# Performance work log

Hardware: AMD Instinct MI355X
Metric: run time of the kernel (lower is better)

## Reference

```python
import jax, jax.numpy as jnp
import numpy as np

B, L, D, H, NL, V, W = 4, 2048, 512, 8, 4, 258, 8
HD = D // H


def setup_inputs() -> dict:
    key = jax.random.key(0)
    ks = jax.random.split(key, 12)
    s = 0.02
    x = jax.random.randint(ks[0], (B, L), 0, V, dtype=jnp.int32)
    patch_lengths = jnp.full((B, 256), W, dtype=jnp.int32)  # sum over patches == L
    emb = jax.random.normal(ks[1], (V, D), jnp.float32) * s
    ent_w = jax.random.normal(ks[2], (D, 1), jnp.float32) * s
    ent_b = jnp.zeros((D,), jnp.float32)
    qkv_w = jax.random.normal(ks[3], (NL, 3 * D, D), jnp.float32) * s
    qkv_b = jnp.zeros((NL, 3 * D), jnp.float32)
    ao_w = jax.random.normal(ks[4], (NL, D, D), jnp.float32) * s
    ao_b = jnp.zeros((NL, D), jnp.float32)
    ln1_s = jnp.ones((NL, D), jnp.float32)
    ln1_b = jnp.zeros((NL, D), jnp.float32)
    ln2_s = jnp.ones((NL, D), jnp.float32)
    ln2_b = jnp.zeros((NL, D), jnp.float32)
    ff1_w = jax.random.normal(ks[5], (NL, 4 * D, D), jnp.float32) * s
    ff1_b = jnp.zeros((NL, 4 * D), jnp.float32)
    ff2_w = jax.random.normal(ks[6], (NL, D, 4 * D), jnp.float32) * s
    ff2_b = jnp.zeros((NL, D), jnp.float32)
    out_w = jax.random.normal(ks[7], (V, D), jnp.float32) * s
    return {"emb": emb, "ent_w": ent_w, "ent_b": ent_b, "qkv_w": qkv_w,
            "qkv_b": qkv_b, "ao_w": ao_w, "ao_b": ao_b, "ln1_s": ln1_s,
            "ln1_b": ln1_b, "ln2_s": ln2_s, "ln2_b": ln2_b, "ff1_w": ff1_w,
            "ff1_b": ff1_b, "ff2_w": ff2_w, "ff2_b": ff2_b, "out_w": out_w,
            "x": x, "patch_lengths": patch_lengths}


def _layernorm(h, scale, bias, eps=1e-5):
    mu = jnp.mean(h, axis=-1, keepdims=True)
    var = jnp.mean(jnp.square(h - mu), axis=-1, keepdims=True)
    return (h - mu) * jax.lax.rsqrt(var + eps) * scale + bias


def _entropy_features(x, dtype):
    # fused sliding-window histogram via one-hot cumsum (replaces per-window bincount loop)
    onehot = jax.nn.one_hot(x, 256, dtype=dtype)            # [B, L, 256]
    c = jnp.cumsum(onehot, axis=1)
    cpad = jnp.concatenate([jnp.zeros_like(c[:, :1]), c], axis=1)
    counts = cpad[:, W:] - cpad[:, :-W]                     # [B, L-W+1, 256]
    p = counts / W
    ent = -jnp.sum(p * jnp.log2(p + 1e-10), axis=-1)        # zero-count terms contribute exactly 0
    full = jnp.zeros(x.shape, dtype).at[:, :x.shape[1] - W + 1].set(ent)
    return full[..., None]                                  # [B, L, 1]


def _block(h, p):
    qkv_w, qkv_b, ao_w, ao_b, l1s, l1b, l2s, l2b, f1w, f1b, f2w, f2b = p
    g = _layernorm(h, l1s, l1b)
    qkv = g @ qkv_w.T + qkv_b                                # [B, L, 3D]
    q, k, v = jnp.split(qkv, 3, axis=-1)
    q = q.reshape(B, L, H, HD)
    k = k.reshape(B, L, H, HD)
    v = v.reshape(B, L, H, HD)
    scores = jnp.einsum('blhd,bmhd->bhlm', q, k) / np.sqrt(HD).astype(h.dtype)
    attn = jax.nn.softmax(scores, axis=-1)
    o = jnp.einsum('bhlm,bmhd->blhd', attn, v).reshape(B, L, D)
    h = h + o @ ao_w.T + ao_b
    g = _layernorm(h, l2s, l2b)
    g = jax.nn.gelu(g @ f1w.T + f1b, approximate=False) @ f2w.T + f2b
    return h + g, None


def reference(emb, ent_w, ent_b, qkv_w, qkv_b, ao_w, ao_b, ln1_s, ln1_b,
              ln2_s, ln2_b, ff1_w, ff1_b, ff2_w, ff2_b, out_w, x, patch_lengths):
    tok = emb[x]                                             # [B, L, D]
    ent = _entropy_features(x, tok.dtype)                    # [B, L, 1]
    ent_emb = ent * ent_w[:, 0] + ent_b                      # Linear(1, D)
    h = tok + ent_emb
    h, _ = jax.lax.scan(_block, h,
                        (qkv_w, qkv_b, ao_w, ao_b, ln1_s, ln1_b,
                         ln2_s, ln2_b, ff1_w, ff1_b, ff2_w, ff2_b))
    # NOTE: the original module's global_transformer/patch-pool branch does not
    # feed the returned logits (dead code); logits come from the local stream h.
    logits = h @ out_w.T                                     # [B, L, V]
    return logits
```

## Files before the change

kernel.cpp:

```cpp
#include <hip/hip_runtime.h>
#include <hip/hip_bf16.h>
#include <math.h>

#define BB 4
#define LL 2048
#define DD 512
#define HH 8
#define NLAYER 4
#define VV 258
#define WW 8
#define HDIM 64
#define MM (BB * LL)
#define VPAD 384

#define C8 0.18033688f

typedef __attribute__((ext_vector_type(8))) short short8v;
typedef __attribute__((ext_vector_type(4))) float float4v;

typedef __attribute__((address_space(3))) unsigned int lds_u32;
typedef const __attribute__((address_space(1))) unsigned int glb_u32;

__device__ __forceinline__ unsigned short f2bf(float x) {
    unsigned int u = __float_as_uint(x);
    unsigned int r = (u + 0x7fffu + ((u >> 16) & 1u)) >> 16;
    return (unsigned short)r;
}
__device__ __forceinline__ float bf2f(unsigned short u) {
    return __uint_as_float((unsigned)u << 16);
}

__device__ __forceinline__ unsigned lds_addr(const void* p) {
    return (unsigned)(size_t)(__attribute__((address_space(3))) const void*)p;
}

#define E0 (NLAYER * 3 * DD * DD)
#define E1 (E0 + NLAYER * DD * DD)
#define E2 (E1 + NLAYER * 4 * DD * DD)
#define E3 (E2 + NLAYER * 4 * DD * DD)
#define E4 (E3 + VPAD * DD)

__global__ __launch_bounds__(256)
void cvt_all_kernel(const float* __restrict__ qkv_w, const float* __restrict__ ao_w,
                    const float* __restrict__ ff1_w, const float* __restrict__ ff2_w,
                    const float* __restrict__ out_w, unsigned short* __restrict__ dst)
{
    int i = (blockIdx.x * 256 + threadIdx.x) * 4;
    float4 v;
    if (i < E0)      v = *reinterpret_cast<const float4*>(qkv_w + i);
    else if (i < E1) v = *reinterpret_cast<const float4*>(ao_w + (i - E0));
    else if (i < E2) v = *reinterpret_cast<const float4*>(ff1_w + (i - E1));
    else if (i < E3) v = *reinterpret_cast<const float4*>(ff2_w + (i - E2));
    else {
        int idx = i - E3;
        if ((idx >> 9) < VV) v = *reinterpret_cast<const float4*>(out_w + idx);
        else                 v = (float4){0.f, 0.f, 0.f, 0.f};
    }
    uint2 pk;
    pk.x = (unsigned)f2bf(v.x) | ((unsigned)f2bf(v.y) << 16);
    pk.y = (unsigned)f2bf(v.z) | ((unsigned)f2bf(v.w) << 16);
    *reinterpret_cast<uint2*>(dst + i) = pk;
}

__global__ __launch_bounds__(256)
void embed_ln_kernel(const int* __restrict__ x,
                     const float* __restrict__ emb,
                     const float* __restrict__ ent_w,
                     const float* __restrict__ ent_b,
                     const float* __restrict__ ln_s,
                     const float* __restrict__ ln_b,
                     unsigned short* __restrict__ h,
                     unsigned short* __restrict__ g)
{
    int w = threadIdx.x >> 6, lane = threadIdx.x & 63;
    int row = blockIdx.x * 4 + w;
    int b = row / LL, l = row % LL;

    float ent = 0.f;
    if (l <= LL - WW) {
        int win[WW];
        #pragma unroll
        for (int i = 0; i < WW; i++) win[i] = x[b * LL + l + i];
        float s = 0.f;
        #pragma unroll
        for (int i = 0; i < WW; i++) {
            if (win[i] < 256) {
                int c = 0;
                #pragma unroll
                for (int j = 0; j < WW; j++) c += (win[j] == win[i]) ? 1 : 0;
                s += log2f((float)c * 0.125f + 1e-10f);
            }
        }
        ent = -s * 0.125f;
    }

    int tok = x[row];
    const float* erow = emb + (size_t)tok * DD + lane * 8;
    float v[8], ew[8], eb[8];
    *reinterpret_cast<float4*>(v)      = *reinterpret_cast<const float4*>(erow);
    *reinterpret_cast<float4*>(v + 4)  = *reinterpret_cast<const float4*>(erow + 4);
    *reinterpret_cast<float4*>(ew)     = *reinterpret_cast<const float4*>(ent_w + lane * 8);
    *reinterpret_cast<float4*>(ew + 4) = *reinterpret_cast<const float4*>(ent_w + lane * 8 + 4);
    *reinterpret_cast<float4*>(eb)     = *reinterpret_cast<const float4*>(ent_b + lane * 8);
    *reinterpret_cast<float4*>(eb + 4) = *reinterpret_cast<const float4*>(ent_b + lane * 8 + 4);

    float sum = 0.f, sq = 0.f;
    #pragma unroll
    for (int i = 0; i < 8; i++) {
        v[i] = v[i] + ent * ew[i] + eb[i];
        sum += v[i]; sq += v[i] * v[i];
    }
    unsigned int hpk[4];
    #pragma unroll
    for (int i = 0; i < 4; i++)
        hpk[i] = (unsigned)f2bf(v[2*i]) | ((unsigned)f2bf(v[2*i+1]) << 16);
    *reinterpret_cast<uint4*>(h + (size_t)row * DD + lane * 8) =
        *reinterpret_cast<const uint4*>(hpk);

    #pragma unroll
    for (int off = 32; off > 0; off >>= 1) {
        sum += __shfl_xor(sum, off);
        sq  += __shfl_xor(sq, off);
    }
    float mu = sum * (1.f / DD);
    float var = sq * (1.f / DD) - mu * mu;
    float rstd = rsqrtf(var + 1e-5f);

    float s8[8], bi[8];
    *reinterpret_cast<float4*>(s8)     = *reinterpret_cast<const float4*>(ln_s + lane * 8);
    *reinterpret_cast<float4*>(s8 + 4) = *reinterpret_cast<const float4*>(ln_s + lane * 8 + 4);
    *reinterpret_cast<float4*>(bi)     = *reinterpret_cast<const float4*>(ln_b + lane * 8);
    *reinterpret_cast<float4*>(bi + 4) = *reinterpret_cast<const float4*>(ln_b + lane * 8 + 4);

    unsigned int pk[4];
    #pragma unroll
    for (int i = 0; i < 4; i++) {
        unsigned short lo = f2bf((v[2*i]   - mu) * rstd * s8[2*i]   + bi[2*i]);
        unsigned short hi = f2bf((v[2*i+1] - mu) * rstd * s8[2*i+1] + bi[2*i+1]);
        pk[i] = (unsigned)lo | ((unsigned)hi << 16);
    }
    *reinterpret_cast<uint4*>(g + (size_t)row * DD + lane * 8) =
        *reinterpret_cast<const uint4*>(pk);
}

__global__ __launch_bounds__(256)
void ln_kernel(const unsigned short* __restrict__ h,
               const float* __restrict__ scale,
               const float* __restrict__ bias,
               unsigned short* __restrict__ g)
{
    int w = threadIdx.x >> 6, lane = threadIdx.x & 63;
    int row = blockIdx.x * 4 + w;

    uint4 raw = *reinterpret_cast<const uint4*>(h + (size_t)row * DD + lane * 8);
    const unsigned* rw = reinterpret_cast<const unsigned*>(&raw);
    float v[8];
    #pragma unroll
    for (int i = 0; i < 4; i++) {
        v[2*i]   = __uint_as_float(rw[i] << 16);
        v[2*i+1] = __uint_as_float(rw[i] & 0xffff0000u);
    }

    float sum = 0.f, sq = 0.f;
    #pragma unroll
    for (int i = 0; i < 8; i++) { sum += v[i]; sq += v[i] * v[i]; }
    #pragma unroll
    for (int off = 32; off > 0; off >>= 1) {
        sum += __shfl_xor(sum, off);
        sq  += __shfl_xor(sq, off);
    }
    float mu = sum * (1.f / DD);
    float var = sq * (1.f / DD) - mu * mu;
    float rstd = rsqrtf(var + 1e-5f);

    float s[8], bi[8];
    *reinterpret_cast<float4*>(s)      = *reinterpret_cast<const float4*>(scale + lane * 8);
    *reinterpret_cast<float4*>(s + 4)  = *reinterpret_cast<const float4*>(scale + lane * 8 + 4);
    *reinterpret_cast<float4*>(bi)     = *reinterpret_cast<const float4*>(bias + lane * 8);
    *reinterpret_cast<float4*>(bi + 4) = *reinterpret_cast<const float4*>(bias + lane * 8 + 4);

    unsigned int pk[4];
    #pragma unroll
    for (int i = 0; i < 4; i++) {
        unsigned short lo = f2bf((v[2*i]   - mu) * rstd * s[2*i]   + bi[2*i]);
        unsigned short hi = f2bf((v[2*i+1] - mu) * rstd * s[2*i+1] + bi[2*i+1]);
        pk[i] = (unsigned)lo | ((unsigned)hi << 16);
    }
    *reinterpret_cast<uint4*>(g + (size_t)row * DD + lane * 8) =
        *reinterpret_cast<const uint4*>(pk);
}

template<bool HAS_BIAS, bool GELU, bool RESID, bool QSCALE, int OMODE, int MT>
__global__ __launch_bounds__(MT * 2)
void gemm_mfma(const unsigned short* __restrict__ A,
               const unsigned short* __restrict__ W,
               const float* __restrict__ bias,
               const unsigned short* __restrict__ resid,
               void* __restrict__ Cv,
               int Nn, int Kk)
{
    constexpr int NW = MT / 32;
    constexpr int BLOADS = 512 / MT;
    constexpr int VMN = 4 + BLOADS;

    __shared__ unsigned short As[2][MT * 64];
    __shared__ unsigned short Bs[2][128 * 64];

    int t = threadIdx.x;
    int w = t >> 6, lane = t & 63;
    int wr = (MT == 128) ? (w >> 1) : 0;
    int wc = (MT == 128) ? (w & 1) : w;
    int l15 = lane & 15, l4 = lane >> 4;
    int m0 = blockIdx.y * MT, n0 = blockIdx.x * 128;

    int lrow = lane >> 3;
    int segp = (lane & 7) ^ lrow;

    float4v acc[4][4];
    #pragma unroll
    for (int i = 0; i < 4; i++)
        #pragma unroll
        for (int j = 0; j < 4; j++)
            acc[i][j] = (float4v){0.f, 0.f, 0.f, 0.f};

    #define STAGE(buf, k0) do {                                                   \
        _Pragma("unroll")                                                         \
        for (int i_ = 0; i_ < 4; i_++) {                                          \
            int r_ = i_ * (NW * 8) + w * 8 + lrow;                                \
            __builtin_amdgcn_global_load_lds(                                     \
                (glb_u32*)(A + (size_t)(m0 + r_) * Kk + (k0) + segp * 8),         \
                (lds_u32*)(As[buf] + i_ * (NW * 512) + w * 512), 16, 0, 0);       \
        }                                                                         \
        _Pragma("unroll")                                                         \
        for (int i_ = 0; i_ < BLOADS; i_++) {                                     \
            int r_ = i_ * (NW * 8) + w * 8 + lrow;                                \
            __builtin_amdgcn_global_load_lds(                                     \
                (glb_u32*)(W + (size_t)(n0 + r_) * Kk + (k0) + segp * 8),         \
                (lds_u32*)(Bs[buf] + i_ * (NW * 512) + w * 512), 16, 0, 0);       \
        } } while (0)

    int nk = Kk >> 6;
    STAGE(0, 0);
    for (int kt = 0; kt < nk; kt++) {
        int cur = kt & 1;
        if (kt + 1 < nk) {
            STAGE(cur ^ 1, (kt + 1) << 6);
            __builtin_amdgcn_sched_barrier(0);
            if constexpr (VMN == 8)  asm volatile("s_waitcnt vmcnt(8)");
            else                     asm volatile("s_waitcnt vmcnt(12)");
            __builtin_amdgcn_sched_barrier(0);
        } else {
            __builtin_amdgcn_sched_barrier(0);
            asm volatile("s_waitcnt vmcnt(0)");
            __builtin_amdgcn_sched_barrier(0);
        }
        __builtin_amdgcn_s_barrier();

        const char* asb = (const char*)As[cur];
        const char* bsb = (const char*)Bs[cur];
        #pragma unroll
        for (int kc = 0; kc < 2; kc++) {
            short8v af[4], bfr[4];
            #pragma unroll
            for (int mf = 0; mf < 4; mf++) {
                int row = wr * 64 + mf * 16 + l15;
                int off = (row * 128 + kc * 64 + l4 * 16) ^ ((row & 7) << 4);
                af[mf] = *reinterpret_cast<const short8v*>(asb + off);
            }
            #pragma unroll
            for (int nf = 0; nf < 4; nf++) {
                int row = wc * 64 + nf * 16 + l15;
                int off = (row * 128 + kc * 64 + l4 * 16) ^ ((row & 7) << 4);
                bfr[nf] = *reinterpret_cast<const short8v*>(bsb + off);
            }
            #pragma unroll
            for (int mf = 0; mf < 4; mf++)
                #pragma unroll
                for (int nf = 0; nf < 4; nf++)
                    acc[mf][nf] = __builtin_amdgcn_mfma_f32_16x16x32_bf16(
                        af[mf], bfr[nf], acc[mf][nf], 0, 0, 0);
        }
        __builtin_amdgcn_s_barrier();
    }
    #undef STAGE

    #pragma unroll
    for (int mf = 0; mf < 4; mf++)
        #pragma unroll
        for (int nf = 0; nf < 4; nf++)
            #pragma unroll
            for (int r = 0; r < 4; r++) {
                int m = m0 + wr * 64 + mf * 16 + l4 * 4 + r;
                int n = n0 + wc * 64 + nf * 16 + l15;
                if (n < Nn) {
                    float v = acc[mf][nf][r];
                    if (HAS_BIAS) v += bias[n];
                    if (GELU) {
                        float a = 0.044715f * v * v;
                        float u = fminf(fmaf(a, v, v) * 2.3022077f, 80.f);
                        float e = __builtin_amdgcn_exp2f(u);
                        v = v * e * __builtin_amdgcn_rcpf(e + 1.f);
                    }
                    if (RESID)    v += bf2f(resid[(size_t)m * Nn + n]);
                    if (QSCALE && n < DD) v *= C8;
                    if (OMODE == 1)
                        ((unsigned short*)Cv)[(size_t)m * Nn + n] = f2bf(v);
                    else
                        ((float*)Cv)[(size_t)m * Nn + n] = v;
                }
            }
}

__global__ __launch_bounds__(512, 2)
void attn_mfma(const unsigned short* __restrict__ qkv, unsigned short* __restrict__ o)
{
    __shared__ unsigned short Kl[2][128 * 64];
    __shared__ unsigned short Vs[2][128 * 64];
    __shared__ float Scl[8][2][16];

    int t = threadIdx.x, w = t >> 6, lane = t & 63;
    int l15 = lane & 15, l4 = lane >> 4;

    int flat = blockIdx.x;
    int swz = (flat & 7) * 32 + (flat >> 3);
    int qt = swz & 7, hh = (swz >> 3) & 7, b = swz >> 6;

    int q0 = qt * 256 + w * 32;
    const int RS = 3 * DD;

    short8v qfA[2], qfB[2];
    #pragma unroll
    for (int dh = 0; dh < 2; dh++) {
        size_t addrA = (size_t)(b * LL + q0 + l15) * RS + hh * HDIM + dh * 32 + l4 * 8;
        qfA[dh] = *reinterpret_cast<const short8v*>(qkv + addrA);
        qfB[dh] = *reinterpret_cast<const short8v*>(qkv + addrA + 16 * RS);
    }

    float4v oA[4], oB[4];
    #pragma unroll
    for (int dt = 0; dt < 4; dt++) {
        oA[dt] = (float4v){0.f, 0.f, 0.f, 0.f};
        oB[dt] = (float4v){0.f, 0.f, 0.f, 0.f};
    }
    float lA = 0.f, lB = 0.f;

    int lrow8 = lane >> 3;
    int ksegp = (lane & 7) ^ lrow8;
    int rho = w * 8 + lrow8;
    int kappa = ((rho >> 5) << 5) | (((rho >> 4) & 1) << 2)
              | (((rho >> 2) & 3) << 3) | (rho & 3);
    int vrow = ((t >> 5) << 2) | ((t >> 1) & 3);
    int vseg = (((t >> 3) & 3) << 1) | (t & 1);
    const unsigned short* kgl = qkv + (size_t)(b * LL + kappa) * RS
                              + hh * HDIM + DD + ksegp * 8;
    const unsigned short* vgl = qkv + (size_t)(b * LL + vrow) * RS
                              + hh * HDIM + 2 * DD + vseg * 8;
    const int halfstep = 64 * RS;
    const int step = 128 * RS;

    #define ASTAGE(buf) do {                                                      \
        __builtin_amdgcn_global_load_lds((glb_u32*)kgl,                           \
            (lds_u32*)(Kl[buf] + w * 512), 16, 0, 0);                             \
        __builtin_amdgcn_global_load_lds((glb_u32*)(kgl + halfstep),              \
            (lds_u32*)(Kl[buf] + 4096 + w * 512), 16, 0, 0);                      \
        __builtin_amdgcn_global_load_lds((glb_u32*)vgl,                           \
            (lds_u32*)(Vs[buf] + w * 512), 16, 0, 0);                             \
        __builtin_amdgcn_global_load_lds((glb_u32*)(vgl + halfstep),              \
            (lds_u32*)(Vs[buf] + 4096 + w * 512), 16, 0, 0);                      \
        kgl += step; vgl += step; } while (0)

    unsigned vtrbase = lds_addr(Vs) + ((lane >> 4) << 10)
                     + (((lane >> 2) & 3) << 5) + ((lane & 3) << 3);

    ASTAGE(0);
    asm volatile("s_waitcnt vmcnt(0)");
    __syncthreads();

    for (int kb = 0; kb < LL / 128; kb++) {
        int cur = kb & 1;
        if (kb + 1 < LL / 128) ASTAGE(cur ^ 1);

        #pragma unroll
        for (int hf = 0; hf < 2; hf++) {
            const char* klc = (const char*)Kl[cur] + hf * 8192;
            unsigned vb = vtrbase + cur * 16384 + hf * 8192;

            float4v sA[4], sB[4];
            __builtin_amdgcn_s_setprio(1);
            #pragma unroll
            for (int nt = 0; nt < 4; nt++) {
                sA[nt] = (float4v){0.f, 0.f, 0.f, 0.f};
                sB[nt] = (float4v){0.f, 0.f, 0.f, 0.f};
                #pragma unroll
                for (int dh = 0; dh < 2; dh++) {
                    int row = nt * 16 + l15;
                    int off = (row * 128 + dh * 64 + l4 * 16) ^ ((row & 7) << 4);
                    short8v kf = *reinterpret_cast<const short8v*>(klc + off);
                    sA[nt] = __builtin_amdgcn_mfma_f32_16x16x32_bf16(kf, qfA[dh], sA[nt], 0, 0, 0);
                    sB[nt] = __builtin_amdgcn_mfma_f32_16x16x32_bf16(kf, qfB[dh], sB[nt], 0, 0, 0);
                }
            }
            __builtin_amdgcn_s_setprio(0);

            unsigned long long a0, a1, a2, a3, a4, a5, a6, a7;
            unsigned long long b0, b1, b2, b3, b4, b5, b6, b7;
            unsigned ab0 = vb, ab1 = vb + 4096;
            asm volatile("ds_read_b64_tr_b16 %0, %1" : "=v"(a0) : "v"(ab0));
            asm volatile("ds_read_b64_tr_b16 %0, %1" : "=v"(a1) : "v"(ab0 + 512));
            asm volatile("ds_read_b64_tr_b16 %0, %1" : "=v"(a2) : "v"(ab0 + 128));
            asm volatile("ds_read_b64_tr_b16 %0, %1" : "=v"(a3) : "v"(ab0 + 640));
            asm volatile("ds_read_b64_tr_b16 %0, %1" : "=v"(a4) : "v"(ab0 + 256));
            asm volatile("ds_read_b64_tr_b16 %0, %1" : "=v"(a5) : "v"(ab0 + 768));
            asm volatile("ds_read_b64_tr_b16 %0, %1" : "=v"(a6) : "v"(ab0 + 384));
            asm volatile("ds_read_b64_tr_b16 %0, %1" : "=v"(a7) : "v"(ab0 + 896));
            asm volatile("ds_read_b64_tr_b16 %0, %1" : "=v"(b0) : "v"(ab1));
            asm volatile("ds_read_b64_tr_b16 %0, %1" : "=v"(b1) : "v"(ab1 + 512));
            asm volatile("ds_read_b64_tr_b16 %0, %1" : "=v"(b2) : "v"(ab1 + 128));
            asm volatile("ds_read_b64_tr_b16 %0, %1" : "=v"(b3) : "v"(ab1 + 640));
            asm volatile("ds_read_b64_tr_b16 %0, %1" : "=v"(b4) : "v"(ab1 + 256));
            asm volatile("ds_read_b64_tr_b16 %0, %1" : "=v"(b5) : "v"(ab1 + 768));
            asm volatile("ds_read_b64_tr_b16 %0, %1" : "=v"(b6) : "v"(ab1 + 384));
            asm volatile("ds_read_b64_tr_b16 %0, %1" : "=v"(b7) : "v"(ab1 + 896));

            union { unsigned u[4]; short8v v; } pf0A, pf1A, pf0B, pf1B;
            {
                float p0 = __builtin_amdgcn_exp2f(sA[0][0]);
                float p1 = __builtin_amdgcn_exp2f(sA[0][1]);
                float p2 = __builtin_amdgcn_exp2f(sA[0][2]);
                float p3 = __builtin_amdgcn_exp2f(sA[0][3]);
                float p4 = __builtin_amdgcn_exp2f(sA[1][0]);
                float p5 = __builtin_amdgcn_exp2f(sA[1][1]);
                float p6 = __builtin_amdgcn_exp2f(sA[1][2]);
                float p7 = __builtin_amdgcn_exp2f(sA[1][3]);
                asm("v_cvt_pk_bf16_f32 %0, %1, %2" : "=v"(pf0A.u[0]) : "v"(p0), "v"(p1));
                asm("v_cvt_pk_bf16_f32 %0, %1, %2" : "=v"(pf0A.u[1]) : "v"(p2), "v"(p3));
                asm("v_cvt_pk_bf16_f32 %0, %1, %2" : "=v"(pf0A.u[2]) : "v"(p4), "v"(p5));
                asm("v_cvt_pk_bf16_f32 %0, %1, %2" : "=v"(pf0A.u[3]) : "v"(p6), "v"(p7));
                float q0_ = __builtin_amdgcn_exp2f(sA[2][0]);
                float q1_ = __builtin_amdgcn_exp2f(sA[2][1]);
                float q2_ = __builtin_amdgcn_exp2f(sA[2][2]);
                float q3_ = __builtin_amdgcn_exp2f(sA[2][3]);
                float q4_ = __builtin_amdgcn_exp2f(sA[3][0]);
                float q5_ = __builtin_amdgcn_exp2f(sA[3][1]);
                float q6_ = __builtin_amdgcn_exp2f(sA[3][2]);
                float q7_ = __builtin_amdgcn_exp2f(sA[3][3]);
                asm("v_cvt_pk_bf16_f32 %0, %1, %2" : "=v"(pf1A.u[0]) : "v"(q0_), "v"(q1_));
                asm("v_cvt_pk_bf16_f32 %0, %1, %2" : "=v"(pf1A.u[1]) : "v"(q2_), "v"(q3_));
                asm("v_cvt_pk_bf16_f32 %0, %1, %2" : "=v"(pf1A.u[2]) : "v"(q4_), "v"(q5_));
                asm("v_cvt_pk_bf16_f32 %0, %1, %2" : "=v"(pf1A.u[3]) : "v"(q6_), "v"(q7_));
                lA += ((p0 + p1) + (p2 + p3)) + ((p4 + p5) + (p6 + p7))
                    + ((q0_ + q1_) + (q2_ + q3_)) + ((q4_ + q5_) + (q6_ + q7_));
            }
            {
                float p0 = __builtin_amdgcn_exp2f(sB[0][0]);
                float p1 = __builtin_amdgcn_exp2f(sB[0][1]);
                float p2 = __builtin_amdgcn_exp2f(sB[0][2]);
                float p3 = __builtin_amdgcn_exp2f(sB[0][3]);
                float p4 = __builtin_amdgcn_exp2f(sB[1][0]);
                float p5 = __builtin_amdgcn_exp2f(sB[1][1]);
                float p6 = __builtin_amdgcn_exp2f(sB[1][2]);
                float p7 = __builtin_amdgcn_exp2f(sB[1][3]);
                asm("v_cvt_pk_bf16_f32 %0, %1, %2" : "=v"(pf0B.u[0]) : "v"(p0), "v"(p1));
                asm("v_cvt_pk_bf16_f32 %0, %1, %2" : "=v"(pf0B.u[1]) : "v"(p2), "v"(p3));
                asm("v_cvt_pk_bf16_f32 %0, %1, %2" : "=v"(pf0B.u[2]) : "v"(p4), "v"(p5));
                asm("v_cvt_pk_bf16_f32 %0, %1, %2" : "=v"(pf0B.u[3]) : "v"(p6), "v"(p7));
                float q0_ = __builtin_amdgcn_exp2f(sB[2][0]);
                float q1_ = __builtin_amdgcn_exp2f(sB[2][1]);
                float q2_ = __builtin_amdgcn_exp2f(sB[2][2]);
                float q3_ = __builtin_amdgcn_exp2f(sB[2][3]);
                float q4_ = __builtin_amdgcn_exp2f(sB[3][0]);
                float q5_ = __builtin_amdgcn_exp2f(sB[3][1]);
                float q6_ = __builtin_amdgcn_exp2f(sB[3][2]);
                float q7_ = __builtin_amdgcn_exp2f(sB[3][3]);
                asm("v_cvt_pk_bf16_f32 %0, %1, %2" : "=v"(pf1B.u[0]) : "v"(q0_), "v"(q1_));
                asm("v_cvt_pk_bf16_f32 %0, %1, %2" : "=v"(pf1B.u[1]) : "v"(q2_), "v"(q3_));
                asm("v_cvt_pk_bf16_f32 %0, %1, %2" : "=v"(pf1B.u[2]) : "v"(q4_), "v"(q5_));
                asm("v_cvt_pk_bf16_f32 %0, %1, %2" : "=v"(pf1B.u[3]) : "v"(q6_), "v"(q7_));
                lB += ((p0 + p1) + (p2 + p3)) + ((p4 + p5) + (p6 + p7))
                    + ((q0_ + q1_) + (q2_ + q3_)) + ((q4_ + q5_) + (q6_ + q7_));
            }

            union { unsigned long long q[2]; short8v v; } u0, u1, u2, u3;
            asm volatile("s_waitcnt lgkmcnt(8)");
            __builtin_amdgcn_sched_barrier(0);
            __builtin_amdgcn_s_setprio(1);
            u0.q[0] = a0; u0.q[1] = a1;
            u1.q[0] = a2; u1.q[1] = a3;
            oA[0] = __builtin_amdgcn_mfma_f32_16x16x32_bf16(pf0A.v, u0.v, oA[0], 0, 0, 0);
            oB[0] = __builtin_amdgcn_mfma_f32_16x16x32_bf16(pf0B.v, u0.v, oB[0], 0, 0, 0);
            oA[1] = __builtin_amdgcn_mfma_f32_16x16x32_bf16(pf0A.v, u1.v, oA[1], 0, 0, 0);
            oB[1] = __builtin_amdgcn_mfma_f32_16x16x32_bf16(pf0B.v, u1.v, oB[1], 0, 0, 0);
            asm volatile("s_waitcnt lgkmcnt(4)");
            __builtin_amdgcn_sched_barrier(0);
            u2.q[0] = a4; u2.q[1] = a5;
            u3.q[0] = a6; u3.q[1] = a7;
            oA[2] = __builtin_amdgcn_mfma_f32_16x16x32_bf16(pf0A.v, u2.v, oA[2], 0, 0, 0);
            oB[2] = __builtin_amdgcn_mfma_f32_16x16x32_bf16(pf0B.v, u2.v, oB[2], 0, 0, 0);
            oA[3] = __builtin_amdgcn_mfma_f32_16x16x32_bf16(pf0A.v, u3.v, oA[3], 0, 0, 0);
            oB[3] = __builtin_amdgcn_mfma_f32_16x16x32_bf16(pf0B.v, u3.v, oB[3], 0, 0, 0);
            asm volatile("s_waitcnt lgkmcnt(0)");
            __builtin_amdgcn_sched_barrier(0);
            u0.q[0] = b0; u0.q[1] = b1;
            u1.q[0] = b2; u1.q[1] = b3;
            u2.q[0] = b4; u2.q[1] = b5;
            u3.q[0] = b6; u3.q[1] = b7;
            oA[0] = __builtin_amdgcn_mfma_f32_16x16x32_bf16(pf1A.v, u0.v, oA[0], 0, 0, 0);
            oB[0] = __builtin_amdgcn_mfma_f32_16x16x32_bf16(pf1B.v, u0.v, oB[0], 0, 0, 0);
            oA[1] = __builtin_amdgcn_mfma_f32_16x16x32_bf16(pf1A.v, u1.v, oA[1], 0, 0, 0);
            oB[1] = __builtin_amdgcn_mfma_f32_16x16x32_bf16(pf1B.v, u1.v, oB[1], 0, 0, 0);
            oA[2] = __builtin_amdgcn_mfma_f32_16x16x32_bf16(pf1A.v, u2.v, oA[2], 0, 0, 0);
            oB[2] = __builtin_amdgcn_mfma_f32_16x16x32_bf16(pf1B.v, u2.v, oB[2], 0, 0, 0);
            oA[3] = __builtin_amdgcn_mfma_f32_16x16x32_bf16(pf1A.v, u3.v, oA[3], 0, 0, 0);
            oB[3] = __builtin_amdgcn_mfma_f32_16x16x32_bf16(pf1B.v, u3.v, oB[3], 0, 0, 0);
            __builtin_amdgcn_s_setprio(0);
        }

        asm volatile("s_waitcnt vmcnt(0)");
        __syncthreads();
    }
    #undef ASTAGE

    float ltA = lA, ltB = lB;
    ltA += __shfl_xor(ltA, 16); ltA += __shfl_xor(ltA, 32);
    ltB += __shfl_xor(ltB, 16); ltB += __shfl_xor(ltB, 32);
    if (l4 == 0) { Scl[w][0][l15] = 1.f / ltA; Scl[w][1][l15] = 1.f / ltB; }
    float4 ivA = *reinterpret_cast<const float4*>(&Scl[w][0][l4 * 4]);
    float4 ivB = *reinterpret_cast<const float4*>(&Scl[w][1][l4 * 4]);
    float invA[4] = {ivA.x, ivA.y, ivA.z, ivA.w};
    float invB[4] = {ivB.x, ivB.y, ivB.z, ivB.w};
    #pragma unroll
    for (int r = 0; r < 4; r++) {
        int qgA = q0 + l4 * 4 + r;
        #pragma unroll
        for (int dt = 0; dt < 4; dt++) {
            o[(size_t)(b * LL + qgA) * DD + hh * HDIM + dt * 16 + l15] =
                f2bf(oA[dt][r] * invA[r]);
            o[(size_t)(b * LL + qgA + 16) * DD + hh * HDIM + dt * 16 + l15] =
                f2bf(oB[dt][r] * invB[r]);
        }
    }
}

extern "C" void kernel_launch(void* const* d_in, const int* in_sizes, int n_in,
                              void* d_out, int out_size, void* d_ws, size_t ws_size,
                              hipStream_t stream)
{
    const float* emb    = (const float*)d_in[0];
    const float* ent_w  = (const float*)d_in[1];
    const float* ent_b  = (const float*)d_in[2];
    const float* qkv_w  = (const float*)d_in[3];
    const float* qkv_b  = (const float*)d_in[4];
    const float* ao_w   = (const float*)d_in[5];
    const float* ao_b   = (const float*)d_in[6];
    const float* ln1_s  = (const float*)d_in[7];
    const float* ln1_b  = (const float*)d_in[8];
    const float* ln2_s  = (const float*)d_in[9];
    const float* ln2_b  = (const float*)d_in[10];
    const float* ff1_w  = (const float*)d_in[11];
    const float* ff1_b  = (const float*)d_in[12];
    const float* ff2_w  = (const float*)d_in[13];
    const float* ff2_b  = (const float*)d_in[14];
    const float* out_w  = (const float*)d_in[15];
    const int*   x      = (const int*)d_in[16];

    float* out = (float*)d_out;

    const int NQW = NLAYER * 3 * DD * DD;
    const int NAW = NLAYER * DD * DD;
    const int NF1 = NLAYER * 4 * DD * DD;
    const int NF2 = NLAYER * DD * 4 * DD;

    char* p = (char*)d_ws;
    unsigned short* wq  = (unsigned short*)p; p += (size_t)NQW * 2;
    unsigned short* wa  = (unsigned short*)p; p += (size_t)NAW * 2;
    unsigned short* w1  = (unsigned short*)p; p += (size_t)NF1 * 2;
    unsigned short* w2  = (unsigned short*)p; p += (size_t)NF2 * 2;
    unsigned short* wob = (unsigned short*)p; p += (size_t)VPAD * DD * 2;
    unsigned short* h   = (unsigned short*)p; p += (size_t)MM * DD * 2;
    unsigned short* gb  = (unsigned short*)p; p += (size_t)MM * DD * 2;
    unsigned short* ob  = (unsigned short*)p; p += (size_t)MM * DD * 2;
    unsigned short* bb  = (unsigned short*)p; p += (size_t)MM * 4 * DD * 2;

    dim3 blk(256);

    cvt_all_kernel<<<E4 / 1024, blk, 0, stream>>>(qkv_w, ao_w, ff1_w, ff2_w, out_w, wq);

    embed_ln_kernel<<<MM / 4, blk, 0, stream>>>(x, emb, ent_w, ent_b,
                                                ln1_s, ln1_b, h, gb);

    for (int layer = 0; layer < NLAYER; layer++) {
        const unsigned short* qw = wq + (size_t)layer * 3 * DD * DD;
        const unsigned short* aw = wa + (size_t)layer * DD * DD;
        const unsigned short* f1 = w1 + (size_t)layer * 4 * DD * DD;
        const unsigned short* f2 = w2 + (size_t)layer * DD * 4 * DD;
        const float* qb  = qkv_b + (size_t)layer * 3 * DD;
        const float* ab  = ao_b  + (size_t)layer * DD;
        const float* l1s = ln1_s + (size_t)layer * DD;
        const float* l1b = ln1_b + (size_t)layer * DD;
        const float* l2s = ln2_s + (size_t)layer * DD;
        const float* l2b = ln2_b + (size_t)layer * DD;
        const float* f1b = ff1_b + (size_t)layer * 4 * DD;
        const float* f2b = ff2_b + (size_t)layer * DD;

        if (layer > 0)
            ln_kernel<<<MM / 4, blk, 0, stream>>>(h, l1s, l1b, gb);

        {
            dim3 grid((3 * DD) / 128, MM / 128);
            gemm_mfma<true, false, false, true, 1, 128><<<grid, 256, 0, stream>>>(
                gb, qw, qb, nullptr, bb, 3 * DD, DD);
        }

        attn_mfma<<<256, 512, 0, stream>>>(bb, ob);

        {
            dim3 grid(DD / 128, MM / 64);
            gemm_mfma<true, false, true, false, 1, 64><<<grid, 128, 0, stream>>>(
                ob, aw, ab, h, h, DD, DD);
        }

        ln_kernel<<<MM / 4, blk, 0, stream>>>(h, l2s, l2b, gb);

        {
            dim3 grid((4 * DD) / 128, MM / 128);
            gemm_mfma<true, true, false, false, 1, 128><<<grid, 256, 0, stream>>>(
                gb, f1, f1b, nullptr, bb, 4 * DD, DD);
        }

        {
            dim3 grid(DD / 128, MM / 64);
            gemm_mfma<true, false, true, false, 1, 64><<<grid, 128, 0, stream>>>(
                bb, f2, f2b, h, h, DD, 4 * DD);
        }
    }

    {
        dim3 grid(VPAD / 128, MM / 64);
        gemm_mfma<false, false, false, false, 0, 64><<<grid, 128, 0, stream>>>(
            h, wob, nullptr, nullptr, out, VV, DD);
    }
}
```

Before: 720.6 us.

## Split attention blocks into 128-query tiles with four waves each

The attention kernel now launches 512 blocks of 256 threads instead of 256 blocks of 512 threads, so each block covers 128 queries rather than 256. Each wave issues twice as many global-to-LDS loads per K/V stage to fill the same 128-key tiles. This gives more blocks to spread across the 256 CUs and a smaller per-block footprint. The cost is that each block re-reads K/V for only half as many queries, which doubles K/V global traffic.

```diff
diff --git a/kernel.cpp b/kernel.cpp
--- a/kernel.cpp
+++ b/kernel.cpp
@@ -311,21 +311,21 @@
             }
 }
 
-__global__ __launch_bounds__(512, 2)
+__global__ __launch_bounds__(256, 2)
 void attn_mfma(const unsigned short* __restrict__ qkv, unsigned short* __restrict__ o)
 {
     __shared__ unsigned short Kl[2][128 * 64];
     __shared__ unsigned short Vs[2][128 * 64];
-    __shared__ float Scl[8][2][16];
+    __shared__ float Scl[4][2][16];
 
     int t = threadIdx.x, w = t >> 6, lane = t & 63;
     int l15 = lane & 15, l4 = lane >> 4;
 
     int flat = blockIdx.x;
-    int swz = (flat & 7) * 32 + (flat >> 3);
-    int qt = swz & 7, hh = (swz >> 3) & 7, b = swz >> 6;
-
-    int q0 = qt * 256 + w * 32;
+    int swz = (flat & 7) * 64 + (flat >> 3);
+    int qt = swz & 15, hh = (swz >> 4) & 7, b = swz >> 7;
+
+    int q0 = qt * 128 + w * 32;
     const int RS = 3 * DD;
 
     short8v qfA[2], qfB[2];
@@ -346,27 +346,35 @@
 
     int lrow8 = lane >> 3;
     int ksegp = (lane & 7) ^ lrow8;
-    int rho = w * 8 + lrow8;
-    int kappa = ((rho >> 5) << 5) | (((rho >> 4) & 1) << 2)
-              | (((rho >> 2) & 3) << 3) | (rho & 3);
-    int vrow = ((t >> 5) << 2) | ((t >> 1) & 3);
-    int vseg = (((t >> 3) & 3) << 1) | (t & 1);
-    const unsigned short* kgl = qkv + (size_t)(b * LL + kappa) * RS
+    int rho0 = w * 16 + lrow8;
+    int kap0 = ((rho0 >> 5) << 5) | (((rho0 >> 4) & 1) << 2)
+             | (((rho0 >> 2) & 3) << 3) | (rho0 & 3);
+    int c0 = w * 64 + lane;
+    int vr0 = ((c0 >> 5) << 2) | ((c0 >> 1) & 3);
+    int vs0 = (((c0 >> 3) & 3) << 1) | (c0 & 1);
+    const unsigned short* kgl = qkv + (size_t)(b * LL + kap0) * RS
                               + hh * HDIM + DD + ksegp * 8;
-    const unsigned short* vgl = qkv + (size_t)(b * LL + vrow) * RS
-                              + hh * HDIM + 2 * DD + vseg * 8;
-    const int halfstep = 64 * RS;
+    const unsigned short* vgl = qkv + (size_t)(b * LL + vr0) * RS
+                              + hh * HDIM + 2 * DD + vs0 * 8;
     const int step = 128 * RS;
 
     #define ASTAGE(buf) do {                                                      \
         __builtin_amdgcn_global_load_lds((glb_u32*)kgl,                           \
-            (lds_u32*)(Kl[buf] + w * 512), 16, 0, 0);                             \
-        __builtin_amdgcn_global_load_lds((glb_u32*)(kgl + halfstep),              \
-            (lds_u32*)(Kl[buf] + 4096 + w * 512), 16, 0, 0);                      \
+            (lds_u32*)(Kl[buf] + w * 1024), 16, 0, 0);                            \
+        __builtin_amdgcn_global_load_lds((glb_u32*)(kgl + 16 * RS),               \
+            (lds_u32*)(Kl[buf] + w * 1024 + 512), 16, 0, 0);                      \
+        __builtin_amdgcn_global_load_lds((glb_u32*)(kgl + 64 * RS),               \
+            (lds_u32*)(Kl[buf] + 4096 + w * 1024), 16, 0, 0);                     \
+        __builtin_amdgcn_global_load_lds((glb_u32*)(kgl + 80 * RS),               \
+            (lds_u32*)(Kl[buf] + 4096 + w * 1024 + 512), 16, 0, 0);               \
         __builtin_amdgcn_global_load_lds((glb_u32*)vgl,                           \
             (lds_u32*)(Vs[buf] + w * 512), 16, 0, 0);                             \
-        __builtin_amdgcn_global_load_lds((glb_u32*)(vgl + halfstep),              \
+        __builtin_amdgcn_global_load_lds((glb_u32*)(vgl + 32 * RS),               \
+            (lds_u32*)(Vs[buf] + 2048 + w * 512), 16, 0, 0);                      \
+        __builtin_amdgcn_global_load_lds((glb_u32*)(vgl + 64 * RS),               \
             (lds_u32*)(Vs[buf] + 4096 + w * 512), 16, 0, 0);                      \
+        __builtin_amdgcn_global_load_lds((glb_u32*)(vgl + 96 * RS),               \
+            (lds_u32*)(Vs[buf] + 6144 + w * 512), 16, 0, 0);                      \
         kgl += step; vgl += step; } while (0)
 
     unsigned vtrbase = lds_addr(Vs) + ((lane >> 4) << 10)
@@ -611,7 +619,7 @@
                 gb, qw, qb, nullptr, bb, 3 * DD, DD);
         }
 
-        attn_mfma<<<256, 512, 0, stream>>>(bb, ob);
+        attn_mfma<<<512, 256, 0, stream>>>(bb, ob);
 
         {
             dim3 grid(DD / 128, MM / 64);
```

New measurement: 713.2 us. No clear change (-1.0%).
